# Optimization experiments

Hardware: AMD Instinct MI355X
Metric: run time of the kernel (lower is better)

Reference implementation:

```python
import jax, jax.numpy as jnp
import numpy as np

SIZE = 8
STRIDES = (4, 8, 16)
QSCALE = 0.25
QMIN, QMAX = -32768, 32767  # qint16


def fake_quant(x):
    # QuantStub with FixedScaleObserver scale=0.25, qint16
    return jnp.clip(jnp.round(x / QSCALE), QMIN, QMAX) * QSCALE


def roi_align(f, rois, size):
    """torchvision.ops.RoIAlign(output_size=size, spatial_scale=1, sampling_ratio=1, aligned=False).
    f: [N,C,H,W], rois: [A,5] = (batch_idx, x1, y1, x2, y2) -> [A,C,size,size]."""
    N, C, H, W = f.shape
    b = rois[:, 0].astype(jnp.int32)
    x1, y1, x2, y2 = rois[:, 1], rois[:, 2], rois[:, 3], rois[:, 4]
    roi_w = jnp.maximum(x2 - x1, 1.0)
    roi_h = jnp.maximum(y2 - y1, 1.0)
    centers = jnp.arange(size, dtype=f.dtype) + 0.5  # sampling_ratio=1 -> bin center
    y = y1[:, None] + centers[None, :] * (roi_h / size)[:, None]  # [A,S]
    x = x1[:, None] + centers[None, :] * (roi_w / size)[:, None]  # [A,S]

    def prep(c, L):
        valid = (c >= -1.0) & (c <= L)
        c = jnp.maximum(c, 0.0)
        low0 = jnp.floor(c).astype(jnp.int32)
        hi_edge = low0 >= L - 1
        low = jnp.where(hi_edge, L - 1, low0)
        high = jnp.where(hi_edge, L - 1, low0 + 1)
        c = jnp.where(hi_edge, jnp.asarray(L - 1, c.dtype), c)
        frac = c - low.astype(c.dtype)
        return low, high, frac, valid

    yl, yh, fy, vy = prep(y, H)
    xl, xh, fx, vx = prep(x, W)

    ff = f.transpose(0, 2, 3, 1).reshape(N * H * W, C)  # channels-last flat for gather

    def gather(yy, xx):
        idx = (b[:, None, None] * H + yy[:, :, None]) * W + xx[:, None, :]  # [A,S,S]
        return ff[idx]  # [A,S,S,C]

    wy0 = (1.0 - fy)[:, :, None, None]
    wy1 = fy[:, :, None, None]
    wx0 = (1.0 - fx)[:, None, :, None]
    wx1 = fx[:, None, :, None]
    val = (gather(yl, xl) * wy0 * wx0 + gather(yl, xh) * wy0 * wx1
           + gather(yh, xl) * wy1 * wx0 + gather(yh, xh) * wy1 * wx1)
    mask = (vy[:, :, None] & vx[:, None, :])[..., None]
    val = jnp.where(mask, val, 0.0)
    return val.transpose(0, 3, 1, 2)  # [A,C,S,S]


def generate_rois(pixel, batch_index, size):
    bi = batch_index.astype(pixel.dtype)[:, None]
    rois = []
    for s in STRIDES:
        tl = jnp.maximum(pixel / s - size / 2.0, 0.0)
        br = jnp.maximum(pixel / s + size / 2.0, 0.0)
        rois.append(fake_quant(jnp.concatenate([bi, tl, br], axis=-1)))
    return rois


def setup_inputs() -> dict:
    key = jax.random.key(0)
    k0, k1, k2, kp, kb = jax.random.split(key, 5)
    f0 = jax.random.normal(k0, (4, 64, 256, 256), jnp.float32)
    f1 = jax.random.normal(k1, (4, 64, 128, 128), jnp.float32)
    f2 = jax.random.normal(k2, (4, 64, 64, 64), jnp.float32)
    pixel = jax.random.uniform(kp, (4096, 2), jnp.float32) * 1008.0  # raster-map coords
    batch_index = jax.random.randint(kb, (4096,), 0, 4, jnp.int32)
    return {"f0": f0, "f1": f1, "f2": f2, "pixel": pixel, "batch_index": batch_index}


def reference(f0, f1, f2, pixel, batch_index):
    rois = generate_rois(pixel, batch_index, SIZE)
    feats = [roi_align(f, r, SIZE) for f, r in zip((f0, f1, f2), rois)]
    return jnp.concatenate(feats, axis=1)  # [A, sum(C_i), SIZE, SIZE]
```

## Files before the change

### kernel.cpp

```cpp
#include <hip/hip_runtime.h>


#define NCH 64

typedef unsigned int   u32;
typedef unsigned short u16;
typedef float  vf4 __attribute__((ext_vector_type(4)));
typedef u32    vu2 __attribute__((ext_vector_type(2)));

__device__ __forceinline__ float fake_quant(float v) {
    float r = rintf(v * 4.0f);
    r = fminf(fmaxf(r, -32768.0f), 32767.0f);
    return r * 0.25f;
}

struct Prep { int lo, hi; float fr; bool valid; };
__device__ __forceinline__ Prep prep(float c, int L) {
    Prep r;
    r.valid = (c >= -1.0f) && (c <= (float)L);
    c = fmaxf(c, 0.0f);
    const int l0 = (int)floorf(c);
    const bool he = (l0 >= L - 1);
    r.lo = he ? (L - 1) : l0;
    r.hi = he ? (L - 1) : (l0 + 1);
    r.fr = (he ? (float)(L - 1) : c) - (float)r.lo;
    return r;
}

__device__ __forceinline__ u16 f2bf(float x) {
    u32 u = __float_as_uint(x);
    u += 0x7FFFu + ((u >> 16) & 1u);
    return (u16)(u >> 16);
}
__device__ __forceinline__ float bflo(u32 w) { return __uint_as_float(w << 16); }
__device__ __forceinline__ float bfhi(u32 w) { return __uint_as_float(w & 0xFFFF0000u); }

__global__ __launch_bounds__(256) void nchw_to_nhwc_bf16(
    const float* __restrict__ f0, const float* __restrict__ f1,
    const float* __restrict__ f2, u16* __restrict__ n0,
    u16* __restrict__ n1, u16* __restrict__ n2)
{
    __shared__ float tile[64][65];
    const int t = threadIdx.x;
    const int b = blockIdx.y;
    const int g = blockIdx.x;
    const float* src; u16* dst; int HW; int tl;
    if (g < 1024)      { src = f0; dst = n0; HW = 65536; tl = g; }
    else if (g < 1280) { src = f1; dst = n1; HW = 16384; tl = g - 1024; }
    else               { src = f2; dst = n2; HW = 4096;  tl = g - 1280; }
    const int hw0 = tl * 64;
    const float* __restrict__ s = src + (size_t)b * 64 * HW + hw0;
    vu2* __restrict__ d = (vu2*)(dst + ((size_t)b * HW + hw0) * 64);

    const int xq = (t & 15) * 4;
    const int cb = t >> 4;
    #pragma unroll
    for (int k = 0; k < 4; ++k) {
        const int c = k * 16 + cb;
        const vf4 v = __builtin_nontemporal_load(
            (const vf4*)(s + (size_t)c * HW + xq));
        tile[c][xq + 0] = v.x;
        tile[c][xq + 1] = v.y;
        tile[c][xq + 2] = v.z;
        tile[c][xq + 3] = v.w;
    }
    __syncthreads();

    #pragma unroll
    for (int k = 0; k < 4; ++k) {
        const int idx = k * 256 + t;
        const int pos = idx >> 4;
        const int c2  = idx & 15;
        vu2 w;
        w.x = (u32)f2bf(tile[4 * c2 + 0][pos])
            | ((u32)f2bf(tile[4 * c2 + 1][pos]) << 16);
        w.y = (u32)f2bf(tile[4 * c2 + 2][pos])
            | ((u32)f2bf(tile[4 * c2 + 3][pos]) << 16);
        __builtin_nontemporal_store(w, d + pos * 16 + c2);
    }
}

__global__ __launch_bounds__(256) void cropper_qat_bf16(
    const u16* __restrict__ g0, const u16* __restrict__ g1,
    const u16* __restrict__ g2, const float* __restrict__ pixel,
    const int* __restrict__ bidx, float* __restrict__ out)
{
    __shared__ uint4 tile[81 * 8];

    const int a   = blockIdx.x;
    const int lvl = blockIdx.y;

    const float inv_s = (lvl == 0) ? 0.25f : (lvl == 1) ? 0.125f : 0.0625f;
    const int   L     = (lvl == 0) ? 256   : (lvl == 1) ? 128    : 64;
    const u16* __restrict__ f = (lvl == 0) ? g0 : (lvl == 1) ? g1 : g2;

    const int   b  = bidx[a];
    const float px = pixel[2 * a];
    const float py = pixel[2 * a + 1];

    const float x1 = fake_quant(fmaxf(px * inv_s - 4.0f, 0.0f));
    const float y1 = fake_quant(fmaxf(py * inv_s - 4.0f, 0.0f));
    const float x2 = fake_quant(fmaxf(px * inv_s + 4.0f, 0.0f));
    const float y2 = fake_quant(fmaxf(py * inv_s + 4.0f, 0.0f));

    const float binw = fmaxf(x2 - x1, 1.0f) * 0.125f;
    const float binh = fmaxf(y2 - y1, 1.0f) * 0.125f;

    const int y_lo = prep(y1 + 0.5f * binh, L).lo;
    const int x_lo = prep(x1 + 0.5f * binw, L).lo;

    const int tid = threadIdx.x;

    {
        const u16* __restrict__ fbase =
            f + ((size_t)b * L * L + (size_t)y_lo * L + x_lo) * NCH;
        #pragma unroll
        for (int it = 0; it < 3; ++it) {
            const int g = tid + it * 256;
            if (g < 648) {
                const int ly  = g / 72;
                const int rem = g - ly * 72;
                const int pos = ly * 9 + (rem >> 3);
                const int c   = rem & 7;
                const uint4 v = *(const uint4*)(fbase + (size_t)ly * L * NCH + rem * 8);
                tile[pos * 8 + (c ^ (pos & 7))] = v;
            }
        }
    }
    __syncthreads();

    const int p  = tid & 63;
    const int i  = p >> 3;
    const int j  = p & 7;
    const int c0 = tid >> 6;

    const Prep py_ = prep(y1 + ((float)i + 0.5f) * binh, L);
    const Prep px_ = prep(x1 + ((float)j + 0.5f) * binw, L);
    const bool valid = py_.valid && px_.valid;

    const float wy0 = 1.0f - py_.fr, wy1 = py_.fr;
    const float wx0 = 1.0f - px_.fr, wx1 = px_.fr;
    const float w00 = wy0 * wx0, w01 = wy0 * wx1;
    const float w10 = wy1 * wx0, w11 = wy1 * wx1;

    const int r0 = (py_.lo - y_lo) * 9;
    const int r1 = (py_.hi - y_lo) * 9;
    const int pos00 = r0 + (px_.lo - x_lo);
    const int pos01 = r0 + (px_.hi - x_lo);
    const int pos10 = r1 + (px_.lo - x_lo);
    const int pos11 = r1 + (px_.hi - x_lo);

    float r[16];
    #pragma unroll
    for (int k = 0; k < 16; ++k) r[k] = 0.0f;

    #define CORNER(POS, W) {                                                  \
        const uint4 qa = tile[(POS) * 8 + ((2 * c0)     ^ ((POS) & 7))];      \
        const uint4 qb = tile[(POS) * 8 + ((2 * c0 + 1) ^ ((POS) & 7))];      \
        r[0]  += bflo(qa.x) * (W); r[1]  += bfhi(qa.x) * (W);                 \
        r[2]  += bflo(qa.y) * (W); r[3]  += bfhi(qa.y) * (W);                 \
        r[4]  += bflo(qa.z) * (W); r[5]  += bfhi(qa.z) * (W);                 \
        r[6]  += bflo(qa.w) * (W); r[7]  += bfhi(qa.w) * (W);                 \
        r[8]  += bflo(qb.x) * (W); r[9]  += bfhi(qb.x) * (W);                 \
        r[10] += bflo(qb.y) * (W); r[11] += bfhi(qb.y) * (W);                 \
        r[12] += bflo(qb.z) * (W); r[13] += bfhi(qb.z) * (W);                 \
        r[14] += bflo(qb.w) * (W); r[15] += bfhi(qb.w) * (W); }

    CORNER(pos00, w00)
    CORNER(pos01, w01)
    CORNER(pos10, w10)
    CORNER(pos11, w11)
    #undef CORNER

    float* __restrict__ outp =
        out + ((size_t)a * 192 + (size_t)lvl * NCH + (size_t)c0 * 16) * 64 + p;
    #pragma unroll
    for (int k = 0; k < 16; ++k)
        __builtin_nontemporal_store(valid ? r[k] : 0.0f, outp + (size_t)k * 64);
}

__global__ __launch_bounds__(256) void cropper_qat_nchw(
    const float* __restrict__ f0, const float* __restrict__ f1,
    const float* __restrict__ f2, const float* __restrict__ pixel,
    const int* __restrict__ bidx, float* __restrict__ out)
{
    const int a   = blockIdx.x;
    const int lvl = blockIdx.y;
    const float inv_s = (lvl == 0) ? 0.25f : (lvl == 1) ? 0.125f : 0.0625f;
    const int   L     = (lvl == 0) ? 256   : (lvl == 1) ? 128    : 64;
    const float* __restrict__ f = (lvl == 0) ? f0 : (lvl == 1) ? f1 : f2;

    const int   b  = bidx[a];
    const float px = pixel[2 * a];
    const float py = pixel[2 * a + 1];
    const float x1 = fake_quant(fmaxf(px * inv_s - 4.0f, 0.0f));
    const float y1 = fake_quant(fmaxf(py * inv_s - 4.0f, 0.0f));
    const float x2 = fake_quant(fmaxf(px * inv_s + 4.0f, 0.0f));
    const float y2 = fake_quant(fmaxf(py * inv_s + 4.0f, 0.0f));
    const float binw = fmaxf(x2 - x1, 1.0f) * 0.125f;
    const float binh = fmaxf(y2 - y1, 1.0f) * 0.125f;

    const int tid = threadIdx.x;
    const int p = tid & 63, i = p >> 3, j = p & 7, c0 = tid >> 6;

    const Prep py_ = prep(y1 + ((float)i + 0.5f) * binh, L);
    const Prep px_ = prep(x1 + ((float)j + 0.5f) * binw, L);
    const bool valid = py_.valid && px_.valid;
    const float wy0 = 1.0f - py_.fr, wy1 = py_.fr;
    const float wx0 = 1.0f - px_.fr, wx1 = px_.fr;
    const float w00 = wy0 * wx0, w01 = wy0 * wx1, w10 = wy1 * wx0, w11 = wy1 * wx1;

    const size_t HW = (size_t)L * L;
    const float* __restrict__ fb = f + (size_t)b * NCH * HW;
    const int o00 = py_.lo * L + px_.lo, o01 = py_.lo * L + px_.hi;
    const int o10 = py_.hi * L + px_.lo, o11 = py_.hi * L + px_.hi;
    float* __restrict__ outp = out + ((size_t)a * 192 + (size_t)lvl * NCH) * 64 + p;

    #pragma unroll 4
    for (int c = c0; c < NCH; c += 4) {
        const float* __restrict__ fc = fb + (size_t)c * HW;
        float val = ((fc[o00] * w00 + fc[o01] * w01) + fc[o10] * w10) + fc[o11] * w11;
        outp[(size_t)c * 64] = valid ? val : 0.0f;
    }
}

extern "C" void kernel_launch(void* const* d_in, const int* in_sizes, int n_in,
                              void* d_out, int out_size, void* d_ws, size_t ws_size,
                              hipStream_t stream) {
    const float* f0    = (const float*)d_in[0];
    const float* f1    = (const float*)d_in[1];
    const float* f2    = (const float*)d_in[2];
    const float* pixel = (const float*)d_in[3];
    const int*   bidx  = (const int*)d_in[4];
    float* out = (float*)d_out;
    const int A = in_sizes[4];

    const size_t NEED = (size_t)(16777216 + 4194304 + 1048576) * 2 + 131072;
    if (ws_size >= NEED) {
        u16* n0 = (u16*)d_ws;
        u16* n1 = n0 + 16777216;
        u16* n2 = n1 + 4194304;
        nchw_to_nhwc_bf16<<<dim3(1344, 4), 256, 0, stream>>>(f0, f1, f2, n0, n1, n2);
        cropper_qat_bf16<<<dim3(A, 3), 256, 0, stream>>>(n0, n1, n2, pixel, bidx, out);
    } else {
        cropper_qat_nchw<<<dim3(A, 3), 256, 0, stream>>>(f0, f1, f2, pixel, bidx, out);
    }
}
```

Measured before the change: 75.99 us.

## Remap threads to 4 pixels x 4 channels for vectorized float4 output stores

Each thread now handles four adjacent output columns and four channels instead of one pixel and sixteen channels. The bf16 tile reads become 8-byte loads, and results are written as float4 nontemporal stores instead of scalar stores. The goal is fewer store instructions and better-coalesced wide writes to the NCHW output, which dominates traffic. In exchange there are more LDS read instructions per thread and the x-interpolation setup is recomputed four times.

```diff
diff --git a/kernel.cpp b/kernel.cpp
--- a/kernel.cpp
+++ b/kernel.cpp
@@ -129,54 +129,60 @@
     }
     __syncthreads();
 
-    const int p  = tid & 63;
-    const int i  = p >> 3;
-    const int j  = p & 7;
-    const int c0 = tid >> 6;
+    const int s     = tid & 15;
+    const int cg    = tid >> 4;
+    const int i     = s >> 1;
+    const int j0    = (s & 1) * 4;
+    const int chunk = cg >> 1;
+    const int half  = cg & 1;
+
+    const vu2* __restrict__ tl2 = (const vu2*)tile;
 
     const Prep py_ = prep(y1 + ((float)i + 0.5f) * binh, L);
-    const Prep px_ = prep(x1 + ((float)j + 0.5f) * binw, L);
-    const bool valid = py_.valid && px_.valid;
-
-    const float wy0 = 1.0f - py_.fr, wy1 = py_.fr;
-    const float wx0 = 1.0f - px_.fr, wx1 = px_.fr;
-    const float w00 = wy0 * wx0, w01 = wy0 * wx1;
-    const float w10 = wy1 * wx0, w11 = wy1 * wx1;
-
     const int r0 = (py_.lo - y_lo) * 9;
     const int r1 = (py_.hi - y_lo) * 9;
-    const int pos00 = r0 + (px_.lo - x_lo);
-    const int pos01 = r0 + (px_.hi - x_lo);
-    const int pos10 = r1 + (px_.lo - x_lo);
-    const int pos11 = r1 + (px_.hi - x_lo);
-
-    float r[16];
-    #pragma unroll
-    for (int k = 0; k < 16; ++k) r[k] = 0.0f;
-
-    #define CORNER(POS, W) {                                                  \
-        const uint4 qa = tile[(POS) * 8 + ((2 * c0)     ^ ((POS) & 7))];      \
-        const uint4 qb = tile[(POS) * 8 + ((2 * c0 + 1) ^ ((POS) & 7))];      \
-        r[0]  += bflo(qa.x) * (W); r[1]  += bfhi(qa.x) * (W);                 \
-        r[2]  += bflo(qa.y) * (W); r[3]  += bfhi(qa.y) * (W);                 \
-        r[4]  += bflo(qa.z) * (W); r[5]  += bfhi(qa.z) * (W);                 \
-        r[6]  += bflo(qa.w) * (W); r[7]  += bfhi(qa.w) * (W);                 \
-        r[8]  += bflo(qb.x) * (W); r[9]  += bfhi(qb.x) * (W);                 \
-        r[10] += bflo(qb.y) * (W); r[11] += bfhi(qb.y) * (W);                 \
-        r[12] += bflo(qb.z) * (W); r[13] += bfhi(qb.z) * (W);                 \
-        r[14] += bflo(qb.w) * (W); r[15] += bfhi(qb.w) * (W); }
-
-    CORNER(pos00, w00)
-    CORNER(pos01, w01)
-    CORNER(pos10, w10)
-    CORNER(pos11, w11)
-    #undef CORNER
+    const float wy0 = 1.0f - py_.fr, wy1 = py_.fr;
+
+    float acc[4][4];
+    #pragma unroll
+    for (int q = 0; q < 4; ++q) {
+        const Prep px_ = prep(x1 + ((float)(j0 + q) + 0.5f) * binw, L);
+        const bool valid = py_.valid && px_.valid;
+        const float wx0 = 1.0f - px_.fr, wx1 = px_.fr;
+        const float w00 = wy0 * wx0, w01 = wy0 * wx1;
+        const float w10 = wy1 * wx0, w11 = wy1 * wx1;
+        const int cx0 = px_.lo - x_lo, cx1 = px_.hi - x_lo;
+        const int p00 = r0 + cx0, p01 = r0 + cx1;
+        const int p10 = r1 + cx0, p11 = r1 + cx1;
+
+        #define LD(P) tl2[(P) * 16 + ((chunk ^ ((P) & 7)) * 2 + half)]
+        const vu2 a00 = LD(p00);
+        const vu2 a01 = LD(p01);
+        const vu2 a10 = LD(p10);
+        const vu2 a11 = LD(p11);
+        #undef LD
+
+        const float v00[4] = {bflo(a00.x), bfhi(a00.x), bflo(a00.y), bfhi(a00.y)};
+        const float v01[4] = {bflo(a01.x), bfhi(a01.x), bflo(a01.y), bfhi(a01.y)};
+        const float v10[4] = {bflo(a10.x), bfhi(a10.x), bflo(a10.y), bfhi(a10.y)};
+        const float v11[4] = {bflo(a11.x), bfhi(a11.x), bflo(a11.y), bfhi(a11.y)};
+
+        #pragma unroll
+        for (int k = 0; k < 4; ++k) {
+            const float val = v00[k] * w00 + v01[k] * w01
+                            + v10[k] * w10 + v11[k] * w11;
+            acc[q][k] = valid ? val : 0.0f;
+        }
+    }
 
     float* __restrict__ outp =
-        out + ((size_t)a * 192 + (size_t)lvl * NCH + (size_t)c0 * 16) * 64 + p;
-    #pragma unroll
-    for (int k = 0; k < 16; ++k)
-        __builtin_nontemporal_store(valid ? r[k] : 0.0f, outp + (size_t)k * 64);
+        out + ((size_t)a * 192 + (size_t)lvl * NCH + (size_t)cg * 4) * 64 + s * 4;
+    #pragma unroll
+    for (int k = 0; k < 4; ++k) {
+        vf4 f4;
+        f4.x = acc[0][k]; f4.y = acc[1][k]; f4.z = acc[2][k]; f4.w = acc[3][k];
+        __builtin_nontemporal_store(f4, (vf4*)(outp + (size_t)k * 64));
+    }
 }
 
 __global__ __launch_bounds__(256) void cropper_qat_nchw(
```

Measured after the change: 76.93 us. Within noise of the previous version (+1.2%).
